# Performance work log

Hardware: AMD Instinct MI355X
Metric: run time of the kernel (lower is better)

## Reference

```python
import jax, jax.numpy as jnp
from jax import lax
import numpy as np

V, D, H, CO = 50000, 300, 512, 100
B, S, W = 64, 32, 128


def setup_inputs() -> dict:
    key = jax.random.key(0)
    ks = jax.random.split(key, 24)
    sc = 0.1  # mimic uniform(-0.1, 0.1)-style small init; keeps tanh unsaturated
    inp = {
        "paragraphs": jax.random.randint(ks[0], (B, S, W), 0, V, dtype=jnp.int64),
        "embed_table": jax.random.normal(ks[1], (V, D), jnp.float32),
        "conv_w3": jax.random.normal(ks[2], (CO, 1, 3, D), jnp.float32) * 0.05,
        "conv_b3": jax.random.normal(ks[3], (CO,), jnp.float32) * sc,
        "conv_w4": jax.random.normal(ks[4], (CO, 1, 4, D), jnp.float32) * 0.05,
        "conv_b4": jax.random.normal(ks[5], (CO,), jnp.float32) * sc,
        "conv_w5": jax.random.normal(ks[6], (CO, 1, 5, D), jnp.float32) * 0.05,
        "conv_b5": jax.random.normal(ks[7], (CO,), jnp.float32) * sc,
        "proj_w": jax.random.normal(ks[8], (300, 300), jnp.float32) * sc,
        "proj_b": jax.random.normal(ks[9], (300,), jnp.float32) * sc,
        "init_w": jax.random.normal(ks[10], (H, 300), jnp.float32) * sc,
        "init_b": jax.random.normal(ks[11], (H,), jnp.float32) * sc,
        "w_ih_f": jax.random.normal(ks[12], (H, 300), jnp.float32) * sc,
        "w_hh_f": jax.random.normal(ks[13], (H, H), jnp.float32) * sc,
        "b_ih_f": jax.random.normal(ks[14], (H,), jnp.float32) * sc,
        "b_hh_f": jax.random.normal(ks[15], (H,), jnp.float32) * sc,
        "w_ih_b": jax.random.normal(ks[16], (H, 300), jnp.float32) * sc,
        "w_hh_b": jax.random.normal(ks[17], (H, H), jnp.float32) * sc,
        "b_ih_b": jax.random.normal(ks[18], (H,), jnp.float32) * sc,
        "b_hh_b": jax.random.normal(ks[19], (H,), jnp.float32) * sc,
        "cls_w": jax.random.normal(ks[20], (5, 2 * H), jnp.float32) * sc,
        "cls_b": jax.random.normal(ks[21], (5,), jnp.float32) * sc,
    }
    return inp


def _cnn_text(tok, embed_table, conv_params):
    # tok: (N, W) int ids -> (N, 3*CO) sentence features (dropout = eval identity)
    emb = embed_table[tok]              # (N, W, D)
    x = emb[:, None, :, :]              # (N, 1, W, D)
    feats = []
    for w, b in conv_params:
        y = lax.conv_general_dilated(
            x, w, window_strides=(1, 1), padding="VALID",
            dimension_numbers=("NCHW", "OIHW", "NCHW"))  # (N, CO, W-K+1, 1)
        y = jax.nn.relu(y[..., 0] + b[None, :, None])       # (N, CO, W-K+1)
        feats.append(jnp.max(y, axis=2))                    # (N, CO) max-pool over time
    return jnp.concatenate(feats, axis=1)                    # (N, 3*CO)


def reference(paragraphs, embed_table, conv_w3, conv_b3, conv_w4, conv_b4,
              conv_w5, conv_b5, proj_w, proj_b, init_w, init_b,
              w_ih_f, w_hh_f, b_ih_f, b_hh_f, w_ih_b, w_hh_b, b_ih_b, b_hh_b,
              cls_w, cls_b):
    b_, s_, w_ = paragraphs.shape
    tok = paragraphs.reshape(b_ * s_, w_)
    conv_params = [(conv_w3, conv_b3), (conv_w4, conv_b4), (conv_w5, conv_b5)]
    sent = _cnn_text(tok, embed_table, conv_params).reshape(b_, s_, 3 * CO)

    # init_rnn: same init hidden for both directions
    h0 = sent[:, 0, :] @ init_w.T + init_b  # (B, H)

    def step(carry, x_t):
        hf, hb = carry
        xi = x_t @ proj_w.T + proj_b  # (B, 300)
        hf_n = jnp.tanh(xi @ w_ih_f.T + b_ih_f + hf @ w_hh_f.T + b_hh_f)
        hb_n = jnp.tanh(xi @ w_ih_b.T + b_ih_b + hb @ w_hh_b.T + b_hh_b)
        pred = jnp.concatenate([hf_n, hb_n], axis=1) @ cls_w.T + cls_b  # (B, 5)
        return (hf_n, hb_n), pred

    _, preds = lax.scan(step, (h0, h0), jnp.swapaxes(sent, 0, 1))  # (S, B, 5)
    return jnp.swapaxes(preds, 0, 1)  # (B, S, 5)
```

## Files before the change

kernel.cpp:

```cpp
#include <hip/hip_runtime.h>


#define LDSK     304
#define LDSROWB  608
#define LDSBYTES 80256

typedef __bf16   bf16x8 __attribute__((ext_vector_type(8)));
typedef float    f32x16 __attribute__((ext_vector_type(16)));
typedef _Float16 h2v    __attribute__((ext_vector_type(2)));

#define MFMA32(a, b, c) __builtin_amdgcn_mfma_f32_32x32x16_bf16((a), (b), (c), 0, 0, 0)

__global__ void prep_emb(const float* __restrict__ e, __bf16* __restrict__ eh) {
  long i = ((long)blockIdx.x * 256 + threadIdx.x) * 8;
  if (i >= 15000000L) return;
  float4 a = *(const float4*)(e + i);
  float4 b = *(const float4*)(e + i + 4);
  union { __bf16 h[8]; uint4 u; } pk;
  pk.h[0] = (__bf16)a.x; pk.h[1] = (__bf16)a.y; pk.h[2] = (__bf16)a.z; pk.h[3] = (__bf16)a.w;
  pk.h[4] = (__bf16)b.x; pk.h[5] = (__bf16)b.y; pk.h[6] = (__bf16)b.z; pk.h[7] = (__bf16)b.w;
  *(uint4*)(eh + i) = pk.u;
}

__global__ void prep_convw(const float* __restrict__ w3, const float* __restrict__ w4,
                           const float* __restrict__ w5, __bf16* __restrict__ Aw32) {
  int idx = blockIdx.x * 256 + threadIdx.x;
  if (idx >= 48 * 19 * 64 * 8) return;
  int i    = idx & 7;
  int lane = (idx >> 3) & 63;
  int rem  = idx >> 9;
  int ks   = rem % 19, g = rem / 19;
  int kc, cg, j; const float* w;
  if (g < 12)      { kc = 3; cg = g / 3;        j = g % 3;        w = w3; }
  else if (g < 28) { kc = 4; cg = (g - 12) / 4; j = (g - 12) % 4; w = w4; }
  else             { kc = 5; cg = (g - 28) / 5; j = (g - 28) % 5; w = w5; }
  int ch = cg * 32 + (lane & 31);
  int k  = ks * 16 + (lane >> 5) * 8 + i;
  float v = 0.f;
  if (ch < 100 && k < 300) v = w[(ch * kc + j) * 300 + k];
  Aw32[idx] = (__bf16)v;
}

__device__ __forceinline__ unsigned int packf16(float a, float b) {
  h2v h; h[0] = (_Float16)a; h[1] = (_Float16)b;
  return __builtin_bit_cast(unsigned int, h);
}
__global__ void prep_whh(const float* __restrict__ whf, const float* __restrict__ whb,
                         uint4* __restrict__ Wq) {
  int idx = blockIdx.x * 256 + threadIdx.x;
  if (idx >= 2 * 128 * 256) return;
  int dir = idx >> 15;
  int rem = idx & 32767;
  int kq = rem >> 8, tid = rem & 255;
  const float* W = dir ? whb : whf;
  const float* r0 = W + (size_t)tid * 512 + 4 * kq;
  const float* r1 = W + (size_t)(tid + 256) * 512 + 4 * kq;
  uint4 o;
  o.x = packf16(r0[0], r0[1]);
  o.y = packf16(r1[0], r1[1]);
  o.z = packf16(r0[2], r0[3]);
  o.w = packf16(r1[2], r1[3]);
  Wq[idx] = o;
}

__device__ __forceinline__ void conv_chunk32(const char* ldsc, const __bf16* __restrict__ Aw32,
                                             int GB, int kc, int cg0,
                                             const float* __restrict__ bias,
                                             int colbase, int pmax,
                                             float* __restrict__ srow, int lane) {
  const int m32 = lane & 31, hi = lane >> 5;
  f32x16 acc[2][4];
#pragma unroll
  for (int i = 0; i < 2; ++i)
#pragma unroll
    for (int n = 0; n < 4; ++n)
#pragma unroll
      for (int e = 0; e < 16; ++e) acc[i][n][e] = 0.f;

  for (int j = 0; j < kc; ++j) {
    const int row0 = m32 + j;
    const int mask = (row0 & 7) << 4;
    const int rowbyte = row0 * LDSROWB + hi * 16;
    const __bf16* a0 = Aw32 + (size_t)(GB + cg0 * kc + j) * (19 * 512) + lane * 8;
    const __bf16* a1 = Aw32 + (size_t)(GB + (cg0 + 1) * kc + j) * (19 * 512) + lane * 8;
#pragma unroll 2
    for (int ks = 0; ks < 19; ++ks) {
      bf16x8 bf[4];
#pragma unroll
      for (int nt = 0; nt < 4; ++nt) {
        int addr = rowbyte + nt * (32 * LDSROWB) + ks * 32;
        bf[nt] = *(const bf16x8*)(ldsc + (addr ^ mask));
      }
      bf16x8 af0 = *(const bf16x8*)(a0 + ks * 512);
      bf16x8 af1 = *(const bf16x8*)(a1 + ks * 512);
#pragma unroll
      for (int nt = 0; nt < 4; ++nt)
        acc[0][nt] = MFMA32(af0, bf[nt], acc[0][nt]);
#pragma unroll
      for (int nt = 0; nt < 4; ++nt)
        acc[1][nt] = MFMA32(af1, bf[nt], acc[1][nt]);
    }
  }
#pragma unroll
  for (int i = 0; i < 2; ++i) {
    float m[16];
#pragma unroll
    for (int r = 0; r < 16; ++r) m[r] = -3.0e38f;
#pragma unroll
    for (int nt = 0; nt < 4; ++nt) {
      int p = nt * 32 + m32;
      bool valid = (p <= pmax);
#pragma unroll
      for (int r = 0; r < 16; ++r)
        m[r] = fmaxf(m[r], valid ? acc[i][nt][r] : -3.0e38f);
    }
#pragma unroll
    for (int r = 0; r < 16; ++r) {
#pragma unroll
      for (int d = 1; d < 32; d <<= 1) m[r] = fmaxf(m[r], __shfl_xor(m[r], d, 64));
    }
    if (m32 == 0) {
#pragma unroll
      for (int r = 0; r < 16; ++r) {
        int ch = (cg0 + i) * 32 + (r & 3) + 8 * (r >> 2) + 4 * hi;
        if (ch < 100) srow[colbase + ch] = fmaxf(m[r] + bias[ch], 0.f);
      }
    }
  }
}

__global__ void __launch_bounds__(256, 2)
conv_kernel(const int* __restrict__ tok, const __bf16* __restrict__ embh,
            const __bf16* __restrict__ Aw32,
            const float* __restrict__ b3, const float* __restrict__ b4, const float* __restrict__ b5,
            float* __restrict__ sent) {
  extern __shared__ __bf16 lds[];
  char* ldsc = (char*)lds;
  const int sid = blockIdx.x, tid = threadIdx.x;
  const int* t0 = tok + sid * 128;
  const char* eb = (const char*)embh;
  for (int i = tid; i < 4 * 76; i += 256) {
    int r = 128 + i / 76, q = i - (i / 76) * 76;
    *(uint2*)(ldsc + ((r * LDSROWB + q * 8) ^ ((r & 7) << 4))) = (uint2){0u, 0u};
  }
  if (tid < 128) {
    *(uint2*)(ldsc + ((tid * LDSROWB + 600) ^ ((tid & 7) << 4))) = (uint2){0u, 0u};
  }
  for (int i = tid; i < 128 * 75; i += 256) {
    int r = i / 75, q = i - r * 75;
    long tk = (long)t0[r];
    uint2 v = *(const uint2*)(eb + tk * 600L + q * 8);
    *(uint2*)(ldsc + ((r * LDSROWB + q * 8) ^ ((r & 7) << 4))) = v;
  }
  __syncthreads();
  const int wave = tid >> 6, lane = tid & 63;
  float* srow = sent + (size_t)sid * 304;
  switch (wave) {
    case 0:
      conv_chunk32(ldsc, Aw32, 28, 5, 0, b5, 200, 123, srow, lane);
      break;
    case 1:
      conv_chunk32(ldsc, Aw32, 28, 5, 2, b5, 200, 123, srow, lane);
      break;
    case 2:
      conv_chunk32(ldsc, Aw32, 12, 4, 0, b4, 100, 124, srow, lane);
      conv_chunk32(ldsc, Aw32,  0, 3, 0, b3,   0, 125, srow, lane);
      break;
    default:
      conv_chunk32(ldsc, Aw32, 12, 4, 2, b4, 100, 124, srow, lane);
      conv_chunk32(ldsc, Aw32,  0, 3, 2, b3,   0, 125, srow, lane);
      break;
  }
}

__global__ void xigh0_kernel(const float* __restrict__ sent,
                             const float* __restrict__ pw, const float* __restrict__ pb,
                             const float* __restrict__ wf, const float* __restrict__ wb,
                             const float* __restrict__ bif, const float* __restrict__ bhf,
                             const float* __restrict__ bib, const float* __restrict__ bhb,
                             const float* __restrict__ iw, const float* __restrict__ ib,
                             float* __restrict__ G, float* __restrict__ h0) {
  __shared__ float s[8][300];
  __shared__ float xi[8][304];
  const int tid = threadIdx.x;
  if (blockIdx.x < 256) {
    const int rb = blockIdx.x * 8;
    for (int i = tid; i < 8 * 300; i += 256) {
      int r = i / 300, c = i - r * 300;
      s[r][c] = sent[(size_t)(rb + r) * 304 + c];
    }
    __syncthreads();
    for (int o = tid; o < 300; o += 256) {
      const float* w = pw + o * 300;
      float bvv = pb[o];
      float a[8];
#pragma unroll
      for (int r = 0; r < 8; ++r) a[r] = bvv;
      for (int k = 0; k < 300; k += 4) {
        float4 wv = *(const float4*)(w + k);
#pragma unroll
        for (int r = 0; r < 8; ++r)
          a[r] += wv.x * s[r][k] + wv.y * s[r][k + 1] + wv.z * s[r][k + 2] + wv.w * s[r][k + 3];
      }
#pragma unroll
      for (int r = 0; r < 8; ++r) xi[r][o] = a[r];
    }
    __syncthreads();
    for (int o = tid; o < 1024; o += 256) {
      int dir = o >> 9, oo = o & 511;
      const float* w = (dir ? wb : wf) + oo * 300;
      float bvv = dir ? (bib[oo] + bhb[oo]) : (bif[oo] + bhf[oo]);
      float a[8];
#pragma unroll
      for (int r = 0; r < 8; ++r) a[r] = bvv;
      for (int k = 0; k < 300; k += 4) {
        float4 wv = *(const float4*)(w + k);
#pragma unroll
        for (int r = 0; r < 8; ++r)
          a[r] += wv.x * xi[r][k] + wv.y * xi[r][k + 1] + wv.z * xi[r][k + 2] + wv.w * xi[r][k + 3];
      }
#pragma unroll
      for (int r = 0; r < 8; ++r) G[(rb + r) * 1024 + o] = a[r];
    }
  } else {
    const int bb = (blockIdx.x - 256) * 8;
    for (int i = tid; i < 8 * 300; i += 256) {
      int r = i / 300, c = i - r * 300;
      s[r][c] = sent[(size_t)((bb + r) * 32) * 304 + c];
    }
    __syncthreads();
    for (int o = tid; o < 512; o += 256) {
      const float* w = iw + o * 300;
      float bvv = ib[o];
      float a[8];
#pragma unroll
      for (int r = 0; r < 8; ++r) a[r] = bvv;
      for (int k = 0; k < 300; k += 4) {
        float4 wv = *(const float4*)(w + k);
#pragma unroll
        for (int r = 0; r < 8; ++r)
          a[r] += wv.x * s[r][k] + wv.y * s[r][k + 1] + wv.z * s[r][k + 2] + wv.w * s[r][k + 3];
      }
#pragma unroll
      for (int r = 0; r < 8; ++r) h0[(bb + r) * 512 + o] = a[r];
    }
  }
}

#if __has_builtin(__builtin_amdgcn_fdot2)
#define FDOT2(a, b, c) __builtin_amdgcn_fdot2((a), (b), (c), false)
#else
static __device__ __forceinline__ float FDOT2(h2v a, h2v b, float c) {
  return c + (float)a[0] * (float)b[0] + (float)a[1] * (float)b[1];
}
#endif
__device__ __forceinline__ h2v as_h2(unsigned int u) { return __builtin_bit_cast(h2v, u); }

__global__ void __launch_bounds__(1024)
rnn_kernel(const uint4* __restrict__ Wq, const float* __restrict__ G,
           const float* __restrict__ h0, float* __restrict__ H) {
  const int blk = blockIdx.x, tid = threadIdx.x;
  const int dir = blk >> 5, b0 = (blk & 31) * 2;
  const int o = tid & 255, kh = (tid >> 8) & 3;
  __shared__ float hs[2][512];
  __shared__ uint2 h2p[2][128];
  __shared__ float part[4][2][512];
  {
    int c = tid >> 9, oo = tid & 511;
    hs[c][oo] = h0[(b0 + c) * 512 + oo];
  }
  __syncthreads();
  const uint4* W = Wq + (size_t)dir * (128 * 256);
  for (int t = 0; t < 32; ++t) {
    if (tid < 256) {
      int c = tid >> 7, kq = tid & 127;
      h2p[c][kq] = (uint2){packf16(hs[c][4 * kq], hs[c][4 * kq + 1]),
                           packf16(hs[c][4 * kq + 2], hs[c][4 * kq + 3])};
    }
    __syncthreads();
    float a00 = 0.f, a01 = 0.f, a10 = 0.f, a11 = 0.f;
    const int kb = kh * 32;
#pragma unroll 4
    for (int kk = 0; kk < 32; ++kk) {
      int kq = kb + kk;
      uint4 w = W[kq * 256 + o];
      uint2 p0 = h2p[0][kq], p1 = h2p[1][kq];
      a00 = FDOT2(as_h2(w.x), as_h2(p0.x), a00); a00 = FDOT2(as_h2(w.z), as_h2(p0.y), a00);
      a01 = FDOT2(as_h2(w.y), as_h2(p0.x), a01); a01 = FDOT2(as_h2(w.w), as_h2(p0.y), a01);
      a10 = FDOT2(as_h2(w.x), as_h2(p1.x), a10); a10 = FDOT2(as_h2(w.z), as_h2(p1.y), a10);
      a11 = FDOT2(as_h2(w.y), as_h2(p1.x), a11); a11 = FDOT2(as_h2(w.w), as_h2(p1.y), a11);
    }
    part[kh][0][o] = a00; part[kh][0][o + 256] = a01;
    part[kh][1][o] = a10; part[kh][1][o + 256] = a11;
    __syncthreads();
    {
      int c = tid >> 9, oo = tid & 511;
      const float* g = G + (size_t)((b0 + c) * 32 + t) * 1024 + dir * 512;
      float s = g[oo] + ((part[0][c][oo] + part[1][c][oo]) + (part[2][c][oo] + part[3][c][oo]));
      float n = tanhf(s);
      hs[c][oo] = n;
      H[(size_t)((dir * 64 + b0 + c) * 32 + t) * 512 + oo] = n;
    }
    __syncthreads();
  }
}

__global__ void pred_kernel(const float* __restrict__ H, const float* __restrict__ cw,
                            const float* __restrict__ cb, float* __restrict__ out) {
  const int bt = blockIdx.x * 4 + (threadIdx.x >> 6);
  const int lane = threadIdx.x & 63;
  const int b = bt >> 5, t = bt & 31;
  const float* hf = H + ((size_t)(b * 32 + t)) * 512;
  const float* hb = H + ((size_t)((64 + b) * 32 + t)) * 512;
  for (int c = 0; c < 5; ++c) {
    const float* w = cw + c * 1024;
    float a = 0.f;
    for (int o = lane; o < 512; o += 64) a += w[o] * hf[o] + w[512 + o] * hb[o];
#pragma unroll
    for (int d = 32; d; d >>= 1) a += __shfl_down(a, d, 64);
    if (lane == 0) out[bt * 5 + c] = a + cb[c];
  }
}

extern "C" void kernel_launch(void* const* d_in, const int* in_sizes, int n_in,
                              void* d_out, int out_size, void* d_ws, size_t ws_size,
                              hipStream_t stream) {
  const int*   tok  = (const int*)d_in[0];
  const float* emb  = (const float*)d_in[1];
  const float* w3   = (const float*)d_in[2];
  const float* b3   = (const float*)d_in[3];
  const float* w4   = (const float*)d_in[4];
  const float* b4   = (const float*)d_in[5];
  const float* w5   = (const float*)d_in[6];
  const float* b5   = (const float*)d_in[7];
  const float* pw   = (const float*)d_in[8];
  const float* pb   = (const float*)d_in[9];
  const float* iw   = (const float*)d_in[10];
  const float* ib   = (const float*)d_in[11];
  const float* wihf = (const float*)d_in[12];
  const float* whhf = (const float*)d_in[13];
  const float* bihf = (const float*)d_in[14];
  const float* bhhf = (const float*)d_in[15];
  const float* wihb = (const float*)d_in[16];
  const float* whhb = (const float*)d_in[17];
  const float* bihb = (const float*)d_in[18];
  const float* bhhb = (const float*)d_in[19];
  const float* cw   = (const float*)d_in[20];
  const float* cb   = (const float*)d_in[21];
  float* out = (float*)d_out;

  char* ws = (char*)d_ws;
  __bf16* Aw32  = (__bf16*)(ws);
  uint4* Wq     = (uint4*)(ws +  1u * 1024 * 1024);
  float* sent   = (float*)(ws +  2u * 1024 * 1024);
  __bf16* embh  = (__bf16*)(ws + 8u * 1024 * 1024);
  float* G      = (float*)(ws +  8u * 1024 * 1024);
  float* h0     = (float*)(ws + 16u * 1024 * 1024);
  float* H      = (float*)(ws + 17u * 1024 * 1024);

  prep_emb<<<7325, 256, 0, stream>>>(emb, embh);
  prep_convw<<<1824, 256, 0, stream>>>(w3, w4, w5, Aw32);
  prep_whh<<<256, 256, 0, stream>>>(whhf, whhb, Wq);

  hipFuncSetAttribute(reinterpret_cast<const void*>(conv_kernel),
                      hipFuncAttributeMaxDynamicSharedMemorySize, LDSBYTES);
  conv_kernel<<<2048, 256, LDSBYTES, stream>>>(tok, embh, Aw32, b3, b4, b5, sent);

  xigh0_kernel<<<264, 256, 0, stream>>>(sent, pw, pb, wihf, wihb, bihf, bhhf, bihb, bhhb,
                                        iw, ib, G, h0);
  rnn_kernel<<<64, 1024, 0, stream>>>(Wq, G, h0, H);
  pred_kernel<<<512, 256, 0, stream>>>(H, cw, cb, out);
}
```

Baseline: 609.8 us.

## Split conv work across eight waves with one channel group each

The conv kernel grows from 256 to 512 threads. Each wave now computes a single 32-channel group (one accumulator set) instead of two, and the waves are rebalanced: four waves run k=5 and k=3, and four run k=4. This cuts per-wave register use and gives more waves to hide LDS and global latency. In exchange each LDS B-fragment load now feeds only 4 MFMAs instead of 8, so total LDS read traffic doubles. With about 80KB of LDS per block, occupancy is still limited to a couple of blocks per CU.

```diff
diff --git a/kernel.cpp b/kernel.cpp
--- a/kernel.cpp
+++ b/kernel.cpp
@@ -63,26 +63,23 @@
   Wq[idx] = o;
 }
 
-__device__ __forceinline__ void conv_chunk32(const char* ldsc, const __bf16* __restrict__ Aw32,
-                                             int GB, int kc, int cg0,
-                                             const float* __restrict__ bias,
-                                             int colbase, int pmax,
-                                             float* __restrict__ srow, int lane) {
+__device__ __forceinline__ void conv_chunk1(const char* ldsc, const __bf16* __restrict__ Aw32,
+                                            int GB, int kc, int cg,
+                                            const float* __restrict__ bias,
+                                            int colbase, int pmax,
+                                            float* __restrict__ srow, int lane) {
   const int m32 = lane & 31, hi = lane >> 5;
-  f32x16 acc[2][4];
-#pragma unroll
-  for (int i = 0; i < 2; ++i)
-#pragma unroll
-    for (int n = 0; n < 4; ++n)
-#pragma unroll
-      for (int e = 0; e < 16; ++e) acc[i][n][e] = 0.f;
+  f32x16 acc[4];
+#pragma unroll
+  for (int n = 0; n < 4; ++n)
+#pragma unroll
+    for (int e = 0; e < 16; ++e) acc[n][e] = 0.f;
 
   for (int j = 0; j < kc; ++j) {
     const int row0 = m32 + j;
     const int mask = (row0 & 7) << 4;
     const int rowbyte = row0 * LDSROWB + hi * 16;
-    const __bf16* a0 = Aw32 + (size_t)(GB + cg0 * kc + j) * (19 * 512) + lane * 8;
-    const __bf16* a1 = Aw32 + (size_t)(GB + (cg0 + 1) * kc + j) * (19 * 512) + lane * 8;
+    const __bf16* a0 = Aw32 + (size_t)(GB + cg * kc + j) * (19 * 512) + lane * 8;
 #pragma unroll 2
     for (int ks = 0; ks < 19; ++ks) {
       bf16x8 bf[4];
@@ -91,45 +88,38 @@
         int addr = rowbyte + nt * (32 * LDSROWB) + ks * 32;
         bf[nt] = *(const bf16x8*)(ldsc + (addr ^ mask));
       }
-      bf16x8 af0 = *(const bf16x8*)(a0 + ks * 512);
-      bf16x8 af1 = *(const bf16x8*)(a1 + ks * 512);
+      bf16x8 af = *(const bf16x8*)(a0 + ks * 512);
 #pragma unroll
       for (int nt = 0; nt < 4; ++nt)
-        acc[0][nt] = MFMA32(af0, bf[nt], acc[0][nt]);
-#pragma unroll
-      for (int nt = 0; nt < 4; ++nt)
-        acc[1][nt] = MFMA32(af1, bf[nt], acc[1][nt]);
-    }
-  }
-#pragma unroll
-  for (int i = 0; i < 2; ++i) {
-    float m[16];
-#pragma unroll
-    for (int r = 0; r < 16; ++r) m[r] = -3.0e38f;
-#pragma unroll
-    for (int nt = 0; nt < 4; ++nt) {
-      int p = nt * 32 + m32;
-      bool valid = (p <= pmax);
-#pragma unroll
-      for (int r = 0; r < 16; ++r)
-        m[r] = fmaxf(m[r], valid ? acc[i][nt][r] : -3.0e38f);
-    }
+        acc[nt] = MFMA32(af, bf[nt], acc[nt]);
+    }
+  }
+  float m[16];
+#pragma unroll
+  for (int r = 0; r < 16; ++r) m[r] = -3.0e38f;
+#pragma unroll
+  for (int nt = 0; nt < 4; ++nt) {
+    int p = nt * 32 + m32;
+    bool valid = (p <= pmax);
+#pragma unroll
+    for (int r = 0; r < 16; ++r)
+      m[r] = fmaxf(m[r], valid ? acc[nt][r] : -3.0e38f);
+  }
+#pragma unroll
+  for (int r = 0; r < 16; ++r) {
+#pragma unroll
+    for (int d = 1; d < 32; d <<= 1) m[r] = fmaxf(m[r], __shfl_xor(m[r], d, 64));
+  }
+  if (m32 == 0) {
 #pragma unroll
     for (int r = 0; r < 16; ++r) {
-#pragma unroll
-      for (int d = 1; d < 32; d <<= 1) m[r] = fmaxf(m[r], __shfl_xor(m[r], d, 64));
-    }
-    if (m32 == 0) {
-#pragma unroll
-      for (int r = 0; r < 16; ++r) {
-        int ch = (cg0 + i) * 32 + (r & 3) + 8 * (r >> 2) + 4 * hi;
-        if (ch < 100) srow[colbase + ch] = fmaxf(m[r] + bias[ch], 0.f);
-      }
-    }
-  }
-}
-
-__global__ void __launch_bounds__(256, 2)
+      int ch = cg * 32 + (r & 3) + 8 * (r >> 2) + 4 * hi;
+      if (ch < 100) srow[colbase + ch] = fmaxf(m[r] + bias[ch], 0.f);
+    }
+  }
+}
+
+__global__ void __launch_bounds__(512, 4)
 conv_kernel(const int* __restrict__ tok, const __bf16* __restrict__ embh,
             const __bf16* __restrict__ Aw32,
             const float* __restrict__ b3, const float* __restrict__ b4, const float* __restrict__ b5,
@@ -139,14 +129,14 @@
   const int sid = blockIdx.x, tid = threadIdx.x;
   const int* t0 = tok + sid * 128;
   const char* eb = (const char*)embh;
-  for (int i = tid; i < 4 * 76; i += 256) {
+  for (int i = tid; i < 4 * 76; i += 512) {
     int r = 128 + i / 76, q = i - (i / 76) * 76;
     *(uint2*)(ldsc + ((r * LDSROWB + q * 8) ^ ((r & 7) << 4))) = (uint2){0u, 0u};
   }
   if (tid < 128) {
     *(uint2*)(ldsc + ((tid * LDSROWB + 600) ^ ((tid & 7) << 4))) = (uint2){0u, 0u};
   }
-  for (int i = tid; i < 128 * 75; i += 256) {
+  for (int i = tid; i < 128 * 75; i += 512) {
     int r = i / 75, q = i - r * 75;
     long tk = (long)t0[r];
     uint2 v = *(const uint2*)(eb + tk * 600L + q * 8);
@@ -155,21 +145,11 @@
   __syncthreads();
   const int wave = tid >> 6, lane = tid & 63;
   float* srow = sent + (size_t)sid * 304;
-  switch (wave) {
-    case 0:
-      conv_chunk32(ldsc, Aw32, 28, 5, 0, b5, 200, 123, srow, lane);
-      break;
-    case 1:
-      conv_chunk32(ldsc, Aw32, 28, 5, 2, b5, 200, 123, srow, lane);
-      break;
-    case 2:
-      conv_chunk32(ldsc, Aw32, 12, 4, 0, b4, 100, 124, srow, lane);
-      conv_chunk32(ldsc, Aw32,  0, 3, 0, b3,   0, 125, srow, lane);
-      break;
-    default:
-      conv_chunk32(ldsc, Aw32, 12, 4, 2, b4, 100, 124, srow, lane);
-      conv_chunk32(ldsc, Aw32,  0, 3, 2, b3,   0, 125, srow, lane);
-      break;
+  if (wave < 4) {
+    conv_chunk1(ldsc, Aw32, 28, 5, wave, b5, 200, 123, srow, lane);
+    conv_chunk1(ldsc, Aw32,  0, 3, wave, b3,   0, 125, srow, lane);
+  } else {
+    conv_chunk1(ldsc, Aw32, 12, 4, wave - 4, b4, 100, 124, srow, lane);
   }
 }
 
@@ -364,7 +344,7 @@
 
   hipFuncSetAttribute(reinterpret_cast<const void*>(conv_kernel),
                       hipFuncAttributeMaxDynamicSharedMemorySize, LDSBYTES);
-  conv_kernel<<<2048, 256, LDSBYTES, stream>>>(tok, embh, Aw32, b3, b4, b5, sent);
+  conv_kernel<<<2048, 512, LDSBYTES, stream>>>(tok, embh, Aw32, b3, b4, b5, sent);
 
   xigh0_kernel<<<264, 256, 0, stream>>>(sent, pw, pb, wihf, wihb, bihf, bhhf, bihb, bhhb,
                                         iw, ib, G, h0);
```

After: 554.9 us. 9.0% less time.
